# Kernel optimization log

Hardware: AMD Instinct MI355X
Metric: run time of the kernel (lower is better)

The kernel has to match this reference:

```python
import jax, jax.numpy as jnp
import numpy as np
from jax.ops import segment_sum

N_NODES = 100000
N_EDGES = 1600000
D = 128
N_LAYERS = 4
N_GRAPHS = 512
LN_EPS = 1e-5


def setup_inputs() -> dict:
    key = jax.random.key(0)
    ks = jax.random.split(key, 8)
    x = jax.random.normal(ks[0], (N_NODES, D), dtype=jnp.float32)
    edge_index = jax.random.randint(ks[1], (2, N_EDGES), 0, N_NODES, dtype=jnp.int64)
    batch = jnp.sort(jax.random.randint(ks[2], (N_NODES,), 0, N_GRAPHS, dtype=jnp.int64))
    scale = 1.0 / np.sqrt(D)
    Ws = jax.random.normal(ks[3], (N_LAYERS, D, D), dtype=jnp.float32) * scale
    bs = jnp.zeros((N_LAYERS, D), dtype=jnp.float32)
    gammas = jnp.ones((N_LAYERS, D), dtype=jnp.float32)
    betas = jnp.zeros((N_LAYERS, D), dtype=jnp.float32)
    lin_w = jax.random.normal(ks[4], (D, 1), dtype=jnp.float32) * scale
    lin_b = jnp.zeros((1,), dtype=jnp.float32)
    return {"x": x, "edge_index": edge_index, "batch": batch, "Ws": Ws,
            "bs": bs, "gammas": gammas, "betas": betas,
            "lin_w": lin_w, "lin_b": lin_b}


def _gcn_conv(x, W, b, src, dst, deg_inv_sqrt):
    # PyG GCNConv: h = x @ W, then sym-normalized aggregation over A + I, then + bias
    h = x @ W                                   # [N, D]
    coef = deg_inv_sqrt[src] * deg_inv_sqrt[dst]  # [E]
    msg = h[src] * coef[:, None]                # [E, D] gather (memory-bound)
    agg = segment_sum(msg, dst, num_segments=x.shape[0])  # scatter-add
    agg = agg + h * (deg_inv_sqrt * deg_inv_sqrt)[:, None]  # self-loop term
    return agg + b


def _layernorm(x, gamma, beta):
    mu = jnp.mean(x, axis=-1, keepdims=True)
    var = jnp.mean(jnp.square(x - mu), axis=-1, keepdims=True)
    return (x - mu) * jax.lax.rsqrt(var + LN_EPS) * gamma + beta


def reference(x, edge_index, batch, Ws, bs, gammas, betas, lin_w, lin_b):
    n = x.shape[0]
    src, dst = edge_index[0], edge_index[1]
    # degree with self-loops (GCNConv adds self loops by default)
    deg = segment_sum(jnp.ones_like(dst, dtype=x.dtype), dst, num_segments=n) + 1.0
    deg_inv_sqrt = jax.lax.rsqrt(deg)

    h = _gcn_conv(x, Ws[0], bs[0], src, dst, deg_inv_sqrt)
    h = _layernorm(h, gammas[0], betas[0])
    h = jax.nn.relu(h)  # dropout is identity in eval mode
    for i in range(1, N_LAYERS):
        h_prev = h
        h = _gcn_conv(h, Ws[i], bs[i], src, dst, deg_inv_sqrt)
        h = _layernorm(h, gammas[i], betas[i])
        h = h + h_prev
        if i < N_LAYERS - 1:
            h = jax.nn.relu(h)

    # global mean pool over graphs
    sums = segment_sum(h, batch, num_segments=N_GRAPHS)        # [G, D]
    cnts = segment_sum(jnp.ones((n,), h.dtype), batch, num_segments=N_GRAPHS)
    pooled = sums / jnp.maximum(cnts, 1.0)[:, None]
    return pooled @ lin_w + lin_b  # [G, 1]
```

## Files before the change

### kernel.cpp

```cpp
#include <hip/hip_runtime.h>
#include <hip/hip_bf16.h>


typedef __hip_bfloat162 bf2;
typedef __attribute__((ext_vector_type(8))) short short8;
typedef __attribute__((ext_vector_type(4))) float f32x4;

#define P1B 512
#define BSH 7
#define BMSK 127
#define MAXB 3072

__global__ __launch_bounds__(256) void k_p1a(const int* __restrict__ dst,
                                             int* __restrict__ bh,
                                             const float* __restrict__ Ws,
                                             __hip_bfloat16* __restrict__ Wt,
                                             int E, int NB) {
    if (blockIdx.x >= P1B) {
        int i = (blockIdx.x - P1B) * 256 + threadIdx.x;
        int layer = i >> 14;
        int m = i & 16383;
        int j = m & 7;
        int l = (m >> 3) & 63;
        int ckb = m >> 9;
        int kb = ckb & 3;
        int c = ckb >> 2;
        int quad = l >> 4, lr = l & 15;
        int k = kb * 32 + quad * 8 + j;
        int col = c * 16 + lr;
        Wt[i] = __float2bfloat16(Ws[layer * 16384 + k * 128 + col]);
        return;
    }
    __shared__ int h[1024];
    const int tid = threadIdx.x;
    for (int i = tid; i < NB; i += 256) h[i] = 0;
    __syncthreads();
    const int per = (((E + P1B - 1) / P1B) + 3) & ~3;
    const int e0 = blockIdx.x * per, e1 = min(E, e0 + per);
    for (int base = e0 + tid * 4; base < e1; base += 1024) {
        if (base + 4 <= e1) {
            int4 d4 = *(const int4*)(dst + base);
            atomicAdd(&h[d4.x >> BSH], 1);
            atomicAdd(&h[d4.y >> BSH], 1);
            atomicAdd(&h[d4.z >> BSH], 1);
            atomicAdd(&h[d4.w >> BSH], 1);
        } else {
            for (int j = base; j < e1; j++) atomicAdd(&h[dst[j] >> BSH], 1);
        }
    }
    __syncthreads();
    int* out = bh + (size_t)blockIdx.x * NB;
    for (int i = tid; i < NB; i += 256) out[i] = h[i];
}

__global__ __launch_bounds__(256) void k_p1b1(int* __restrict__ bh,
                                              int* __restrict__ btot, int NB) {
    __shared__ int s[256];
    const int b = blockIdx.x, tid = threadIdx.x;
    int v0 = bh[(size_t)(2 * tid) * NB + b];
    int v1 = bh[(size_t)(2 * tid + 1) * NB + b];
    int tsum = v0 + v1;
    s[tid] = tsum;
    __syncthreads();
    for (int off = 1; off < 256; off <<= 1) {
        int t = (tid >= off) ? s[tid - off] : 0;
        __syncthreads();
        s[tid] += t;
        __syncthreads();
    }
    int excl = s[tid] - tsum;
    bh[(size_t)(2 * tid) * NB + b] = excl;
    bh[(size_t)(2 * tid + 1) * NB + b] = excl + v0;
    if (tid == 255) btot[b] = s[255];
}

__global__ __launch_bounds__(256) void k_p1b2(const int* __restrict__ btot,
                                              int* __restrict__ bbase,
                                              int* __restrict__ row_off,
                                              float* __restrict__ gsum,
                                              int NB, int E, int n, int G) {
    __shared__ int s[256];
    const int tid = threadIdx.x;
    int v0 = (4 * tid + 0 < NB) ? btot[4 * tid + 0] : 0;
    int v1 = (4 * tid + 1 < NB) ? btot[4 * tid + 1] : 0;
    int v2 = (4 * tid + 2 < NB) ? btot[4 * tid + 2] : 0;
    int v3 = (4 * tid + 3 < NB) ? btot[4 * tid + 3] : 0;
    int tsum = v0 + v1 + v2 + v3;
    s[tid] = tsum;
    __syncthreads();
    for (int off = 1; off < 256; off <<= 1) {
        int t = (tid >= off) ? s[tid - off] : 0;
        __syncthreads();
        s[tid] += t;
        __syncthreads();
    }
    int excl = s[tid] - tsum;
    if (4 * tid + 0 < NB) bbase[4 * tid + 0] = excl;
    if (4 * tid + 1 < NB) bbase[4 * tid + 1] = excl + v0;
    if (4 * tid + 2 < NB) bbase[4 * tid + 2] = excl + v0 + v1;
    if (4 * tid + 3 < NB) bbase[4 * tid + 3] = excl + v0 + v1 + v2;
    if (tid == 0) row_off[n] = E;
    for (int i = tid; i < G; i += 256) gsum[i] = 0.f;
}

__global__ __launch_bounds__(256) void k_p1c(const int* __restrict__ src,
                                             const int* __restrict__ dst,
                                             const int* __restrict__ bh,
                                             const int* __restrict__ bbase,
                                             unsigned* __restrict__ ebuf,
                                             int E, int NB) {
    __shared__ int cur[1024];
    const int tid = threadIdx.x;
    const int* cb = bh + (size_t)blockIdx.x * NB;
    for (int i = tid; i < NB; i += 256) cur[i] = cb[i] + bbase[i];
    __syncthreads();
    const int per = (((E + P1B - 1) / P1B) + 3) & ~3;
    const int e0 = blockIdx.x * per, e1 = min(E, e0 + per);
    for (int base = e0 + tid * 4; base < e1; base += 1024) {
        if (base + 4 <= e1) {
            int4 d4 = *(const int4*)(dst + base);
            int4 s4 = *(const int4*)(src + base);
            int dd[4] = {d4.x, d4.y, d4.z, d4.w};
            int ss[4] = {s4.x, s4.y, s4.z, s4.w};
#pragma unroll
            for (int j = 0; j < 4; j++) {
                int p = atomicAdd(&cur[dd[j] >> BSH], 1);
                ebuf[p] = ((unsigned)(dd[j] & BMSK) << 17) | (unsigned)ss[j];
            }
        } else {
            for (int j = base; j < e1; j++) {
                int d = dst[j];
                int p = atomicAdd(&cur[d >> BSH], 1);
                ebuf[p] = ((unsigned)(d & BMSK) << 17) | (unsigned)src[j];
            }
        }
    }
}

__global__ __launch_bounds__(256) void k_p2(const unsigned* __restrict__ ebuf,
                                            const int* __restrict__ btot,
                                            const int* __restrict__ bbase,
                                            unsigned* __restrict__ colsrc,
                                            int* __restrict__ row_off,
                                            float* __restrict__ dis, int n) {
    __shared__ unsigned ein[MAXB];
    __shared__ int hist[128];
    __shared__ int scn[256];
    const int b = blockIdx.x, tid = threadIdx.x;
    const int base = bbase[b];
    int sz = btot[b];
    if (sz > MAXB) sz = MAXB;
    if (tid < 128) hist[tid] = 0;
    __syncthreads();
    for (int i = tid; i < sz; i += 256) {
        unsigned v = ebuf[base + i];
        ein[i] = v;
        atomicAdd(&hist[v >> 17], 1);
    }
    __syncthreads();
    const int deg = (tid < 128) ? hist[tid] : 0;
    scn[tid] = deg;
    __syncthreads();
    for (int off = 1; off < 256; off <<= 1) {
        int t = (tid >= off) ? scn[tid - off] : 0;
        __syncthreads();
        scn[tid] += t;
        __syncthreads();
    }
    const int excl = scn[tid] - deg;
    const int node = b * 128 + tid;
    if (tid < 128 && node < n) {
        row_off[node] = base + excl;
        dis[node] = rsqrtf((float)deg + 1.0f);
    }
    if (tid < 128) hist[tid] = excl;
    __syncthreads();
    for (int i = tid; i < sz; i += 256) {
        unsigned v = ein[i];
        int p = atomicAdd(&hist[v >> 17], 1);
        colsrc[base + p] = v & 0x1FFFFu;
    }
}

__global__ __launch_bounds__(256) void k_matmul(const __hip_bfloat16* __restrict__ Xb,
                                                const float* __restrict__ Xf,
                                                const __hip_bfloat16* __restrict__ Wt,
                                                __hip_bfloat16* __restrict__ Hb, int n) {
    __shared__ __align__(16) __hip_bfloat16 sX[64 * 136];
    const int tid = threadIdx.x;
    const int row0 = blockIdx.x * 64;
    if (Xf) {
        for (int i = tid; i < 2048; i += 256) {
            int r = i >> 5, c = i & 31;
            int gr = row0 + r;
            float4 v = make_float4(0.f, 0.f, 0.f, 0.f);
            if (gr < n) v = *(const float4*)(Xf + (size_t)gr * 128 + c * 4);
            union { bf2 h2[2]; uint2 u; } pk;
            pk.h2[0].x = __float2bfloat16(v.x);
            pk.h2[0].y = __float2bfloat16(v.y);
            pk.h2[1].x = __float2bfloat16(v.z);
            pk.h2[1].y = __float2bfloat16(v.w);
            *(uint2*)(sX + r * 136 + c * 4) = pk.u;
        }
    } else {
        for (int i = tid; i < 1024; i += 256) {
            int r = i >> 4, ck = i & 15;
            uint4 v = make_uint4(0, 0, 0, 0);
            int gr = row0 + r;
            if (gr < n) v = *(const uint4*)(Xb + (size_t)gr * 128 + ck * 8);
            *(uint4*)(sX + r * 136 + ck * 8) = v;
        }
    }
    __syncthreads();
    const int w = tid >> 6, l = tid & 63;
    const int quad = l >> 4, lr = l & 15;
    f32x4 acc[8];
#pragma unroll
    for (int c = 0; c < 8; c++) acc[c] = (f32x4){0.f, 0.f, 0.f, 0.f};
    short8 a[4];
#pragma unroll
    for (int kb = 0; kb < 4; kb++)
        a[kb] = *(const short8*)(sX + (w * 16 + lr) * 136 + kb * 32 + quad * 8);
#pragma unroll
    for (int c = 0; c < 8; c++) {
#pragma unroll
        for (int kb = 0; kb < 4; kb++) {
            short8 b = *(const short8*)(Wt + ((c * 4 + kb) * 64 + l) * 8);
            acc[c] = __builtin_amdgcn_mfma_f32_16x16x32_bf16(a[kb], b, acc[c], 0, 0, 0);
        }
    }
#pragma unroll
    for (int c = 0; c < 8; c++)
#pragma unroll
        for (int r = 0; r < 4; r++)
            sX[(w * 16 + quad * 4 + r) * 136 + c * 16 + lr] =
                __float2bfloat16(acc[c][r]);
#pragma unroll
    for (int p = 0; p < 4; p++) {
        int r = p * 4 + quad;
        int gr = row0 + w * 16 + r;
        uint4 v = *(const uint4*)(sX + (w * 16 + r) * 136 + lr * 8);
        if (gr < n) *(uint4*)(Hb + (size_t)gr * 128 + lr * 8) = v;
    }
}

__global__ __launch_bounds__(256) void k_node(const __hip_bfloat16* __restrict__ Hb,
                                              __hip_bfloat16* __restrict__ Xb,
                                              const int* __restrict__ row_off,
                                              const unsigned* __restrict__ colsrc,
                                              const float* __restrict__ dis,
                                              const float* __restrict__ bias,
                                              const float* __restrict__ gamma,
                                              const float* __restrict__ beta,
                                              const float* __restrict__ lin_w,
                                              const int* __restrict__ batch,
                                              float* __restrict__ gsum,
                                              int do_relu, int do_res, int fuse_pool,
                                              int n) {
    __shared__ float spd[16];
    __shared__ int   sbt[16];
    const int wave = threadIdx.x >> 6;
    const int lane = threadIdx.x & 63;
    const int grp = lane >> 4;
    const int sub = lane & 15;
    const int node = blockIdx.x * 16 + wave * 4 + grp;
    const bool vn = node < n;
    const int nd = vn ? node : 0;
    const int e0 = vn ? row_off[node] : 0;
    const int e1 = vn ? row_off[node + 1] : 0;
    const char* hbase = (const char*)Hb;
    const unsigned suboff = (unsigned)(sub << 4);

    float dn = dis[nd];
    uint4 sv = *(const uint4*)(hbase + (((unsigned)nd) << 8) + suboff);

    float acc[8];
#pragma unroll
    for (int k = 0; k < 8; k++) acc[k] = 0.f;

    int e = e0;
    unsigned su[8];
#pragma unroll
    for (int u = 0; u < 8; u++) su[u] = colsrc[(e + u < e1) ? e + u : 0];

    while (__any(e < e1)) {
        uint4 v[8];
        float dv[8];
#pragma unroll
        for (int u = 0; u < 8; u++) {
            v[u] = *(const uint4*)(hbase + (su[u] << 8) + suboff);
            dv[u] = dis[su[u]];
        }
        const int en = e + 8;
        unsigned sn[8];
#pragma unroll
        for (int u = 0; u < 8; u++) sn[u] = colsrc[(en + u < e1) ? en + u : 0];
#pragma unroll
        for (int u = 0; u < 8; u++) {
            float c = (e + u < e1) ? dv[u] * dn : 0.f;
            acc[0] += __uint_as_float(v[u].x << 16) * c;
            acc[1] += __uint_as_float(v[u].x & 0xffff0000u) * c;
            acc[2] += __uint_as_float(v[u].y << 16) * c;
            acc[3] += __uint_as_float(v[u].y & 0xffff0000u) * c;
            acc[4] += __uint_as_float(v[u].z << 16) * c;
            acc[5] += __uint_as_float(v[u].z & 0xffff0000u) * c;
            acc[6] += __uint_as_float(v[u].w << 16) * c;
            acc[7] += __uint_as_float(v[u].w & 0xffff0000u) * c;
        }
#pragma unroll
        for (int u = 0; u < 8; u++) su[u] = sn[u];
        e = en;
    }

    {
        float dn2 = dn * dn;
        acc[0] += __uint_as_float(sv.x << 16) * dn2;
        acc[1] += __uint_as_float(sv.x & 0xffff0000u) * dn2;
        acc[2] += __uint_as_float(sv.y << 16) * dn2;
        acc[3] += __uint_as_float(sv.y & 0xffff0000u) * dn2;
        acc[4] += __uint_as_float(sv.z << 16) * dn2;
        acc[5] += __uint_as_float(sv.z & 0xffff0000u) * dn2;
        acc[6] += __uint_as_float(sv.w << 16) * dn2;
        acc[7] += __uint_as_float(sv.w & 0xffff0000u) * dn2;
    }
    float4 b0 = *(const float4*)(bias + sub * 8);
    float4 b1 = *(const float4*)(bias + sub * 8 + 4);
    acc[0] += b0.x; acc[1] += b0.y; acc[2] += b0.z; acc[3] += b0.w;
    acc[4] += b1.x; acc[5] += b1.y; acc[6] += b1.z; acc[7] += b1.w;

    float s = acc[0] + acc[1] + acc[2] + acc[3] + acc[4] + acc[5] + acc[6] + acc[7];
#pragma unroll
    for (int m = 8; m > 0; m >>= 1) s += __shfl_xor(s, m, 64);
    float mu = s * (1.f / 128.f);
    float vs = 0.f;
#pragma unroll
    for (int k = 0; k < 8; k++) {
        float d = acc[k] - mu;
        acc[k] = d;
        vs += d * d;
    }
#pragma unroll
    for (int m = 8; m > 0; m >>= 1) vs += __shfl_xor(vs, m, 64);
    float rs = rsqrtf(vs * (1.f / 128.f) + 1e-5f);

    float4 g0 = *(const float4*)(gamma + sub * 8);
    float4 g1 = *(const float4*)(gamma + sub * 8 + 4);
    float4 t0 = *(const float4*)(beta + sub * 8);
    float4 t1 = *(const float4*)(beta + sub * 8 + 4);
    float y[8];
    y[0] = acc[0] * rs * g0.x + t0.x;
    y[1] = acc[1] * rs * g0.y + t0.y;
    y[2] = acc[2] * rs * g0.z + t0.z;
    y[3] = acc[3] * rs * g0.w + t0.w;
    y[4] = acc[4] * rs * g1.x + t1.x;
    y[5] = acc[5] * rs * g1.y + t1.y;
    y[6] = acc[6] * rs * g1.z + t1.z;
    y[7] = acc[7] * rs * g1.w + t1.w;

    __hip_bfloat16* xp = Xb + (size_t)node * 128 + sub * 8;
    if (vn && do_res) {
        uint4 rv = *(const uint4*)xp;
        y[0] += __uint_as_float(rv.x << 16);
        y[1] += __uint_as_float(rv.x & 0xffff0000u);
        y[2] += __uint_as_float(rv.y << 16);
        y[3] += __uint_as_float(rv.y & 0xffff0000u);
        y[4] += __uint_as_float(rv.z << 16);
        y[5] += __uint_as_float(rv.z & 0xffff0000u);
        y[6] += __uint_as_float(rv.w << 16);
        y[7] += __uint_as_float(rv.w & 0xffff0000u);
    }

    if (fuse_pool) {
        float4 w0 = *(const float4*)(lin_w + sub * 8);
        float4 w1 = *(const float4*)(lin_w + sub * 8 + 4);
        float pdot = y[0] * w0.x + y[1] * w0.y + y[2] * w0.z + y[3] * w0.w +
                     y[4] * w1.x + y[5] * w1.y + y[6] * w1.z + y[7] * w1.w;
#pragma unroll
        for (int m = 8; m > 0; m >>= 1) pdot += __shfl_xor(pdot, m, 64);
        int slot = wave * 4 + grp;
        if (sub == 0) {
            spd[slot] = vn ? pdot : 0.f;
            sbt[slot] = vn ? batch[node] : -1;
        }
        __syncthreads();
        if (threadIdx.x == 0) {
            int i = 0;
            while (i < 16) {
                int b = sbt[i];
                if (b < 0) { i++; continue; }
                float acc2 = spd[i];
                int j = i + 1;
                while (j < 16 && sbt[j] == b) { acc2 += spd[j]; j++; }
                atomicAdd(&gsum[b], acc2);
                i = j;
            }
        }
    } else if (vn) {
        if (do_relu) {
#pragma unroll
            for (int k = 0; k < 8; k++) y[k] = fmaxf(y[k], 0.f);
        }
        union { bf2 h2[4]; uint4 u; } pk;
        pk.h2[0].x = __float2bfloat16(y[0]); pk.h2[0].y = __float2bfloat16(y[1]);
        pk.h2[1].x = __float2bfloat16(y[2]); pk.h2[1].y = __float2bfloat16(y[3]);
        pk.h2[2].x = __float2bfloat16(y[4]); pk.h2[2].y = __float2bfloat16(y[5]);
        pk.h2[3].x = __float2bfloat16(y[6]); pk.h2[3].y = __float2bfloat16(y[7]);
        *(uint4*)xp = pk.u;
    }
}

__global__ void k_out(const float* __restrict__ gsum, const int* __restrict__ batch,
                      const float* __restrict__ lin_b, float* __restrict__ out,
                      int n, int G) {
    int g = blockIdx.x * blockDim.x + threadIdx.x;
    if (g >= G) return;
    int lo = 0, hi = n;
    while (lo < hi) { int m = (lo + hi) >> 1; if (batch[m] < g) lo = m + 1; else hi = m; }
    int start = lo;
    hi = n;
    while (lo < hi) { int m = (lo + hi) >> 1; if (batch[m] <= g) lo = m + 1; else hi = m; }
    float c = (float)(lo - start);
    out[g] = gsum[g] / fmaxf(c, 1.f) + lin_b[0];
}

extern "C" void kernel_launch(void* const* d_in, const int* in_sizes, int n_in,
                              void* d_out, int out_size, void* d_ws, size_t ws_size,
                              hipStream_t stream) {
    const float* x      = (const float*)d_in[0];
    const int*   eidx   = (const int*)d_in[1];
    const int*   batch  = (const int*)d_in[2];
    const float* Ws     = (const float*)d_in[3];
    const float* bs     = (const float*)d_in[4];
    const float* gammas = (const float*)d_in[5];
    const float* betas  = (const float*)d_in[6];
    const float* lin_w  = (const float*)d_in[7];
    const float* lin_b  = (const float*)d_in[8];
    float* out = (float*)d_out;

    const int n = in_sizes[2];
    const int E = in_sizes[1] / 2;
    const int G = out_size;
    const int NB = (n + BMSK) >> BSH;

    const int* src  = eidx;
    const int* dstp = eidx + E;

    char* w = (char*)d_ws;
    size_t off = 0;
    auto alloc = [&](size_t bytes) {
        void* p = w + off;
        off = (off + bytes + 15) & ~(size_t)15;
        return p;
    };
    int*      bh      = (int*)     alloc((size_t)P1B * NB * 4);
    int*      btot    = (int*)     alloc((size_t)NB * 4);
    int*      bbase   = (int*)     alloc((size_t)NB * 4);
    unsigned* ebuf    = (unsigned*)alloc((size_t)E * 4);
    unsigned* colsrc  = (unsigned*)alloc((size_t)E * 4);
    int*      row_off = (int*)     alloc((size_t)(n + 1) * 4);
    float*    dis     = (float*)   alloc((size_t)n * 4);
    float*    gsum    = (float*)   alloc((size_t)G * 4);
    __hip_bfloat16* hb = (__hip_bfloat16*)alloc((size_t)n * 128 * 2);
    __hip_bfloat16* xb = (__hip_bfloat16*)alloc((size_t)n * 128 * 2);
    __hip_bfloat16* wt = (__hip_bfloat16*)alloc((size_t)4 * 128 * 128 * 2);
    (void)ws_size; (void)n_in;

    k_p1a<<<P1B + 256, 256, 0, stream>>>(dstp, bh, Ws, wt, E, NB);
    k_p1b1<<<NB, 256, 0, stream>>>(bh, btot, NB);
    k_p1b2<<<1, 256, 0, stream>>>(btot, bbase, row_off, gsum, NB, E, n, G);
    k_p1c<<<P1B, 256, 0, stream>>>(src, dstp, bh, bbase, ebuf, E, NB);
    k_p2<<<NB, 256, 0, stream>>>(ebuf, btot, bbase, colsrc, row_off, dis, n);

    for (int layer = 0; layer < 4; layer++) {
        k_matmul<<<(n + 63) / 64, 256, 0, stream>>>(xb, (layer == 0) ? x : nullptr,
                                                    wt + (size_t)layer * 16384, hb, n);
        k_node<<<(n + 15) / 16, 256, 0, stream>>>(hb, xb, row_off, colsrc, dis,
                                                  bs + (size_t)layer * 128,
                                                  gammas + (size_t)layer * 128,
                                                  betas + (size_t)layer * 128,
                                                  lin_w, batch, gsum,
                                                  (layer < 3) ? 1 : 0, (layer > 0) ? 1 : 0,
                                                  (layer == 3) ? 1 : 0, n);
    }
    k_out<<<(G + 255) / 256, 256, 0, stream>>>(gsum, batch, lin_b, out, n, G);
}
```

Baseline: 558.0 us.

## Merge preprocessing kernels and co-schedule first matmul with CSR build

Folds the single-block bucket-base scan into every scatter block, which each redundantly rescan the bucket totals. Block 0 writes bbase. The gsum/row_off initialisation moves into an extra block of the histogram kernel. The layer-0 matmul (fp32 input cast to bf16) runs as extra blocks inside the per-bucket CSR sort kernel, since the two are independent. This removes two kernel launches and lets the small sort kernel overlap with the matmul, at the cost of redundant scan work and shared memory sized to the larger of the two block types.

New measurement: 550.9 us (median of 2 runs). About the same (-1.3%).

```diff
diff --git a/kernel.cpp b/kernel.cpp
--- a/kernel.cpp
+++ b/kernel.cpp
@@ -11,11 +11,18 @@
 #define BMSK 127
 #define MAXB 3072
 
-__global__ __launch_bounds__(256) void k_p1a(const int* __restrict__ dst,
-                                             int* __restrict__ bh,
-                                             const float* __restrict__ Ws,
-                                             __hip_bfloat16* __restrict__ Wt,
-                                             int E, int NB) {
+__global__ __launch_bounds__(256) void k_pA(const int* __restrict__ dst,
+                                            int* __restrict__ bh,
+                                            const float* __restrict__ Ws,
+                                            __hip_bfloat16* __restrict__ Wt,
+                                            int* __restrict__ row_off,
+                                            float* __restrict__ gsum,
+                                            int E, int NB, int n, int G) {
+    if (blockIdx.x >= P1B + 256) {
+        for (int i = threadIdx.x; i < G; i += 256) gsum[i] = 0.f;
+        if (threadIdx.x == 0) row_off[n] = E;
+        return;
+    }
     if (blockIdx.x >= P1B) {
         int i = (blockIdx.x - P1B) * 256 + threadIdx.x;
         int layer = i >> 14;
@@ -53,8 +60,8 @@
     for (int i = tid; i < NB; i += 256) out[i] = h[i];
 }
 
-__global__ __launch_bounds__(256) void k_p1b1(int* __restrict__ bh,
-                                              int* __restrict__ btot, int NB) {
+__global__ __launch_bounds__(256) void k_pB(int* __restrict__ bh,
+                                            int* __restrict__ btot, int NB) {
     __shared__ int s[256];
     const int b = blockIdx.x, tid = threadIdx.x;
     int v0 = bh[(size_t)(2 * tid) * NB + b];
@@ -74,18 +81,24 @@
     if (tid == 255) btot[b] = s[255];
 }
 
-__global__ __launch_bounds__(256) void k_p1b2(const int* __restrict__ btot,
-                                              int* __restrict__ bbase,
-                                              int* __restrict__ row_off,
-                                              float* __restrict__ gsum,
-                                              int NB, int E, int n, int G) {
+__global__ __launch_bounds__(256) void k_pC(const int* __restrict__ src,
+                                            const int* __restrict__ dst,
+                                            const int* __restrict__ bh,
+                                            const int* __restrict__ btot,
+                                            int* __restrict__ bbase,
+                                            unsigned* __restrict__ ebuf,
+                                            int E, int NB) {
+    __shared__ int cur[1024];
     __shared__ int s[256];
     const int tid = threadIdx.x;
-    int v0 = (4 * tid + 0 < NB) ? btot[4 * tid + 0] : 0;
-    int v1 = (4 * tid + 1 < NB) ? btot[4 * tid + 1] : 0;
-    int v2 = (4 * tid + 2 < NB) ? btot[4 * tid + 2] : 0;
-    int v3 = (4 * tid + 3 < NB) ? btot[4 * tid + 3] : 0;
-    int tsum = v0 + v1 + v2 + v3;
+    int v[4];
+    int tsum = 0;
+#pragma unroll
+    for (int j = 0; j < 4; j++) {
+        int idx = 4 * tid + j;
+        v[j] = (idx < NB) ? btot[idx] : 0;
+        tsum += v[j];
+    }
     s[tid] = tsum;
     __syncthreads();
     for (int off = 1; off < 256; off <<= 1) {
@@ -95,24 +108,16 @@
         __syncthreads();
     }
     int excl = s[tid] - tsum;
-    if (4 * tid + 0 < NB) bbase[4 * tid + 0] = excl;
-    if (4 * tid + 1 < NB) bbase[4 * tid + 1] = excl + v0;
-    if (4 * tid + 2 < NB) bbase[4 * tid + 2] = excl + v0 + v1;
-    if (4 * tid + 3 < NB) bbase[4 * tid + 3] = excl + v0 + v1 + v2;
-    if (tid == 0) row_off[n] = E;
-    for (int i = tid; i < G; i += 256) gsum[i] = 0.f;
-}
-
-__global__ __launch_bounds__(256) void k_p1c(const int* __restrict__ src,
-                                             const int* __restrict__ dst,
-                                             const int* __restrict__ bh,
-                                             const int* __restrict__ bbase,
-                                             unsigned* __restrict__ ebuf,
-                                             int E, int NB) {
-    __shared__ int cur[1024];
-    const int tid = threadIdx.x;
+#pragma unroll
+    for (int j = 0; j < 4; j++) {
+        int idx = 4 * tid + j;
+        cur[idx] = excl;
+        if (blockIdx.x == 0 && idx < NB) bbase[idx] = excl;
+        excl += v[j];
+    }
+    __syncthreads();
     const int* cb = bh + (size_t)blockIdx.x * NB;
-    for (int i = tid; i < NB; i += 256) cur[i] = cb[i] + bbase[i];
+    for (int i = tid; i < NB; i += 256) cur[i] += cb[i];
     __syncthreads();
     const int per = (((E + P1B - 1) / P1B) + 3) & ~3;
     const int e0 = blockIdx.x * per, e1 = min(E, e0 + per);
@@ -137,79 +142,117 @@
     }
 }
 
-__global__ __launch_bounds__(256) void k_p2(const unsigned* __restrict__ ebuf,
+__global__ __launch_bounds__(256) void k_pD(const unsigned* __restrict__ ebuf,
                                             const int* __restrict__ btot,
                                             const int* __restrict__ bbase,
                                             unsigned* __restrict__ colsrc,
                                             int* __restrict__ row_off,
-                                            float* __restrict__ dis, int n) {
-    __shared__ unsigned ein[MAXB];
-    __shared__ int hist[128];
-    __shared__ int scn[256];
-    const int b = blockIdx.x, tid = threadIdx.x;
-    const int base = bbase[b];
-    int sz = btot[b];
-    if (sz > MAXB) sz = MAXB;
-    if (tid < 128) hist[tid] = 0;
-    __syncthreads();
-    for (int i = tid; i < sz; i += 256) {
-        unsigned v = ebuf[base + i];
-        ein[i] = v;
-        atomicAdd(&hist[v >> 17], 1);
-    }
-    __syncthreads();
-    const int deg = (tid < 128) ? hist[tid] : 0;
-    scn[tid] = deg;
-    __syncthreads();
-    for (int off = 1; off < 256; off <<= 1) {
-        int t = (tid >= off) ? scn[tid - off] : 0;
-        __syncthreads();
-        scn[tid] += t;
-        __syncthreads();
-    }
-    const int excl = scn[tid] - deg;
-    const int node = b * 128 + tid;
-    if (tid < 128 && node < n) {
-        row_off[node] = base + excl;
-        dis[node] = rsqrtf((float)deg + 1.0f);
-    }
-    if (tid < 128) hist[tid] = excl;
-    __syncthreads();
-    for (int i = tid; i < sz; i += 256) {
-        unsigned v = ein[i];
-        int p = atomicAdd(&hist[v >> 17], 1);
-        colsrc[base + p] = v & 0x1FFFFu;
+                                            float* __restrict__ dis,
+                                            const float* __restrict__ Xf,
+                                            const __hip_bfloat16* __restrict__ Wt,
+                                            __hip_bfloat16* __restrict__ Hb,
+                                            int n, int NB) {
+    __shared__ __align__(16) char smem[64 * 136 * 2];
+    const int tid = threadIdx.x;
+    if (blockIdx.x < (unsigned)NB) {
+        unsigned* ein = (unsigned*)smem;
+        int* hist = (int*)(smem + 12288);
+        int* scn  = (int*)(smem + 12800);
+        const int b = blockIdx.x;
+        const int base = bbase[b];
+        int sz = btot[b];
+        if (sz > MAXB) sz = MAXB;
+        if (tid < 128) hist[tid] = 0;
+        __syncthreads();
+        for (int i = tid; i < sz; i += 256) {
+            unsigned v = ebuf[base + i];
+            ein[i] = v;
+            atomicAdd(&hist[v >> 17], 1);
+        }
+        __syncthreads();
+        const int deg = (tid < 128) ? hist[tid] : 0;
+        scn[tid] = deg;
+        __syncthreads();
+        for (int off = 1; off < 256; off <<= 1) {
+            int t = (tid >= off) ? scn[tid - off] : 0;
+            __syncthreads();
+            scn[tid] += t;
+            __syncthreads();
+        }
+        const int excl = scn[tid] - deg;
+        const int node = b * 128 + tid;
+        if (tid < 128 && node < n) {
+            row_off[node] = base + excl;
+            dis[node] = rsqrtf((float)deg + 1.0f);
+        }
+        if (tid < 128) hist[tid] = excl;
+        __syncthreads();
+        for (int i = tid; i < sz; i += 256) {
+            unsigned v = ein[i];
+            int p = atomicAdd(&hist[v >> 17], 1);
+            colsrc[base + p] = v & 0x1FFFFu;
+        }
+        return;
+    }
+    __hip_bfloat16* sX = (__hip_bfloat16*)smem;
+    const int row0 = (blockIdx.x - NB) * 64;
+    for (int i = tid; i < 2048; i += 256) {
+        int r = i >> 5, c = i & 31;
+        int gr = row0 + r;
+        float4 v = make_float4(0.f, 0.f, 0.f, 0.f);
+        if (gr < n) v = *(const float4*)(Xf + (size_t)gr * 128 + c * 4);
+        union { bf2 h2[2]; uint2 u; } pk;
+        pk.h2[0].x = __float2bfloat16(v.x);
+        pk.h2[0].y = __float2bfloat16(v.y);
+        pk.h2[1].x = __float2bfloat16(v.z);
+        pk.h2[1].y = __float2bfloat16(v.w);
+        *(uint2*)(sX + r * 136 + c * 4) = pk.u;
+    }
+    __syncthreads();
+    const int w = tid >> 6, l = tid & 63;
+    const int quad = l >> 4, lr = l & 15;
+    f32x4 acc[8];
+#pragma unroll
+    for (int c = 0; c < 8; c++) acc[c] = (f32x4){0.f, 0.f, 0.f, 0.f};
+    short8 a[4];
+#pragma unroll
+    for (int kb = 0; kb < 4; kb++)
+        a[kb] = *(const short8*)(sX + (w * 16 + lr) * 136 + kb * 32 + quad * 8);
+#pragma unroll
+    for (int c = 0; c < 8; c++) {
+#pragma unroll
+        for (int kb = 0; kb < 4; kb++) {
+            short8 b = *(const short8*)(Wt + ((c * 4 + kb) * 64 + l) * 8);
+            acc[c] = __builtin_amdgcn_mfma_f32_16x16x32_bf16(a[kb], b, acc[c], 0, 0, 0);
+        }
+    }
+#pragma unroll
+    for (int c = 0; c < 8; c++)
+#pragma unroll
+        for (int r = 0; r < 4; r++)
+            sX[(w * 16 + quad * 4 + r) * 136 + c * 16 + lr] =
+                __float2bfloat16(acc[c][r]);
+#pragma unroll
+    for (int p = 0; p < 4; p++) {
+        int r = p * 4 + quad;
+        int gr = row0 + w * 16 + r;
+        uint4 v = *(const uint4*)(sX + (w * 16 + r) * 136 + lr * 8);
+        if (gr < n) *(uint4*)(Hb + (size_t)gr * 128 + lr * 8) = v;
     }
 }
 
 __global__ __launch_bounds__(256) void k_matmul(const __hip_bfloat16* __restrict__ Xb,
-                                                const float* __restrict__ Xf,
                                                 const __hip_bfloat16* __restrict__ Wt,
                                                 __hip_bfloat16* __restrict__ Hb, int n) {
     __shared__ __align__(16) __hip_bfloat16 sX[64 * 136];
     const int tid = threadIdx.x;
     const int row0 = blockIdx.x * 64;
-    if (Xf) {
-        for (int i = tid; i < 2048; i += 256) {
-            int r = i >> 5, c = i & 31;
-            int gr = row0 + r;
-            float4 v = make_float4(0.f, 0.f, 0.f, 0.f);
-            if (gr < n) v = *(const float4*)(Xf + (size_t)gr * 128 + c * 4);
-            union { bf2 h2[2]; uint2 u; } pk;
-            pk.h2[0].x = __float2bfloat16(v.x);
-            pk.h2[0].y = __float2bfloat16(v.y);
-            pk.h2[1].x = __float2bfloat16(v.z);
-            pk.h2[1].y = __float2bfloat16(v.w);
-            *(uint2*)(sX + r * 136 + c * 4) = pk.u;
-        }
-    } else {
-        for (int i = tid; i < 1024; i += 256) {
-            int r = i >> 4, ck = i & 15;
-            uint4 v = make_uint4(0, 0, 0, 0);
-            int gr = row0 + r;
-            if (gr < n) v = *(const uint4*)(Xb + (size_t)gr * 128 + ck * 8);
-            *(uint4*)(sX + r * 136 + ck * 8) = v;
-        }
+    for (int i = tid; i < 1024; i += 256) {
+        int r = i >> 4, ck = i & 15;
+        uint4 v = make_uint4(0, 0, 0, 0);
+        int gr = row0 + r;
+        if (gr < n) v = *(const uint4*)(Xb + (size_t)gr * 128 + ck * 8);
+        *(uint4*)(sX + r * 136 + ck * 8) = v;
     }
     __syncthreads();
     const int w = tid >> 6, l = tid & 63;
@@ -465,15 +508,19 @@
     __hip_bfloat16* wt = (__hip_bfloat16*)alloc((size_t)4 * 128 * 128 * 2);
     (void)ws_size; (void)n_in;
 
-    k_p1a<<<P1B + 256, 256, 0, stream>>>(dstp, bh, Ws, wt, E, NB);
-    k_p1b1<<<NB, 256, 0, stream>>>(bh, btot, NB);
-    k_p1b2<<<1, 256, 0, stream>>>(btot, bbase, row_off, gsum, NB, E, n, G);
-    k_p1c<<<P1B, 256, 0, stream>>>(src, dstp, bh, bbase, ebuf, E, NB);
-    k_p2<<<NB, 256, 0, stream>>>(ebuf, btot, bbase, colsrc, row_off, dis, n);
+    const int mm_tiles = (n + 63) / 64;
+
+    k_pA<<<P1B + 256 + 1, 256, 0, stream>>>(dstp, bh, Ws, wt, row_off, gsum,
+                                            E, NB, n, G);
+    k_pB<<<NB, 256, 0, stream>>>(bh, btot, NB);
+    k_pC<<<P1B, 256, 0, stream>>>(src, dstp, bh, btot, bbase, ebuf, E, NB);
+    k_pD<<<NB + mm_tiles, 256, 0, stream>>>(ebuf, btot, bbase, colsrc,
+                                            row_off, dis, x, wt, hb, n, NB);
 
     for (int layer = 0; layer < 4; layer++) {
-        k_matmul<<<(n + 63) / 64, 256, 0, stream>>>(xb, (layer == 0) ? x : nullptr,
-                                                    wt + (size_t)layer * 16384, hb, n);
+        if (layer > 0)
+            k_matmul<<<mm_tiles, 256, 0, stream>>>(xb, wt + (size_t)layer * 16384,
+                                                   hb, n);
         k_node<<<(n + 15) / 16, 256, 0, stream>>>(hb, xb, row_off, colsrc, dis,
                                                   bs + (size_t)layer * 128,
                                                   gammas + (size_t)layer * 128,
```
